# Kernel tuning notes

Hardware: AMD Instinct MI355X
Metric: run time of the kernel (lower is better)

The kernel has to match this reference:

```python
import jax, jax.numpy as jnp
import numpy as np

MAX_REL_POS = 16


def relative_position_ids(t, max_pos):
    r = jnp.arange(t)
    dist = jnp.clip(r[None, :] - r[:, None], -max_pos, max_pos)
    return dist + max_pos  # [T, T] in [0, 2*max_pos]


def setup_inputs():
    key = jax.random.key(0)
    ks = jax.random.split(key, 5)
    B, H, T, D = 2, 16, 1024, 64
    V = 2 * MAX_REL_POS + 1  # 33
    q = jax.random.normal(ks[0], (B, H, T, D), dtype=jnp.float32)
    k = jax.random.normal(ks[1], (B, H, T, D), dtype=jnp.float32)
    v = jax.random.normal(ks[2], (B, H, T, D), dtype=jnp.float32)
    embed_k = jax.random.normal(ks[3], (V, D), dtype=jnp.float32)
    embed_v = jax.random.normal(ks[4], (V, D), dtype=jnp.float32)
    mask = jnp.zeros((1, 1, T, T), dtype=jnp.float32)
    return {"q": q, "k": k, "v": v, "embed_k": embed_k, "embed_v": embed_v, "mask": mask}


def reference(q, k, v, embed_k, embed_v, mask):
    T = q.shape[2]
    D = k.shape[-1]
    rel = relative_position_ids(T, MAX_REL_POS)           # [T, T] int
    rel_k = embed_k[rel]                                   # [T, T, D]
    rel_v = embed_v[rel]                                   # [T, T, D]
    # QK^T plus relative-key term (matmul_with_relative_representations, transpose_b=True)
    logits = jnp.einsum('bhqd,bhkd->bhqk', q, k) + jnp.einsum('bhqd,qkd->bhqk', q, rel_k)
    logits = logits * (1.0 / jnp.sqrt(jnp.asarray(D, dtype=logits.dtype)))
    logits = logits + mask * (-1e9)
    attn = jax.nn.softmax(logits, axis=-1)                 # [B, H, T, T]
    out = jnp.einsum('bhqk,bhkd->bhqd', attn, v) + jnp.einsum('bhqk,qkd->bhqd', attn, rel_v)
    return out, attn
```

## Files before the change

### kernel.cpp

```cpp
#include <hip/hip_runtime.h>

#define BHN 32
#define T 1024
#define DD 64
#define TQ 16
#define PST 1032

typedef __attribute__((ext_vector_type(8))) __bf16 bf16x8;
typedef __attribute__((ext_vector_type(8))) unsigned short us8;
typedef __attribute__((ext_vector_type(4))) float f32x4;

struct alignas(16) U4 { unsigned a, b, c, d; };

__device__ __forceinline__ unsigned short f2bf(float x) {
  unsigned u = __builtin_bit_cast(unsigned, x);
  u += 0x7fffu + ((u >> 16) & 1u);
  return (unsigned short)(u >> 16);
}
__device__ __forceinline__ float bf2f(unsigned short h) {
  unsigned u = ((unsigned)h) << 16;
  return __builtin_bit_cast(float, u);
}
__device__ __forceinline__ bf16x8 ld_bf16x8(const unsigned short* p) {
  U4 u = *(const U4*)p;
  return __builtin_bit_cast(bf16x8, u);
}

__global__ __launch_bounds__(256) void prep_conv(
    const float* __restrict__ k, const float* __restrict__ v,
    unsigned short* __restrict__ kbf, unsigned short* __restrict__ vt)
{
  __shared__ float sT[64][66];
  const int bh = blockIdx.y;
  const int tb = blockIdx.x * 64;
  const int t = threadIdx.x;
  const size_t base = (size_t)bh * T * DD + (size_t)tb * DD;

  const float4* ksrc = (const float4*)(k + base);
#pragma unroll
  for (int i = 0; i < 2; ++i) {
    int g = i * 256 + t;
    float4 a = ksrc[g * 2], b = ksrc[g * 2 + 1];
    us8 u;
    u[0] = f2bf(a.x); u[1] = f2bf(a.y); u[2] = f2bf(a.z); u[3] = f2bf(a.w);
    u[4] = f2bf(b.x); u[5] = f2bf(b.y); u[6] = f2bf(b.z); u[7] = f2bf(b.w);
    *(us8*)(kbf + base + (size_t)g * 8) = u;
  }

  const float4* v4 = (const float4*)(v + base);
#pragma unroll
  for (int i = 0; i < 4; ++i) {
    int g = i * 256 + t;
    float4 x = v4[g];
    int tl = g >> 4;
    int d0 = (g & 15) * 4;
    sT[d0][tl] = x.x; sT[d0 + 1][tl] = x.y; sT[d0 + 2][tl] = x.z; sT[d0 + 3][tl] = x.w;
  }
  __syncthreads();

  unsigned short* vdst = vt + (size_t)bh * DD * T + tb;
#pragma unroll
  for (int i = 0; i < 2; ++i) {
    int item = i * 256 + t;
    int dd = item >> 3;
    int kk0 = (item & 7) * 8;
    float2 x0 = *(const float2*)&sT[dd][kk0];
    float2 x1 = *(const float2*)&sT[dd][kk0 + 2];
    float2 x2 = *(const float2*)&sT[dd][kk0 + 4];
    float2 x3 = *(const float2*)&sT[dd][kk0 + 6];
    us8 u;
    u[0] = f2bf(x0.x); u[1] = f2bf(x0.y); u[2] = f2bf(x1.x); u[3] = f2bf(x1.y);
    u[4] = f2bf(x2.x); u[5] = f2bf(x2.y); u[6] = f2bf(x3.x); u[7] = f2bf(x3.y);
    *(us8*)(vdst + (size_t)dd * T + kk0) = u;
  }
}

__global__ __launch_bounds__(256, 4) void attn_main(
    const float* __restrict__ q, const unsigned short* __restrict__ kbf,
    const unsigned short* __restrict__ vt, const float* __restrict__ ek,
    const float* __restrict__ ev, const float* __restrict__ mask,
    float* __restrict__ out, float* __restrict__ attn)
{
  __shared__ unsigned short sP[TQ * PST];
  __shared__ float sQek[TQ][33];
  __shared__ float sDiag[TQ][31];
  __shared__ float sRS[4][TQ];
  __shared__ float sRB[4][TQ];
  __shared__ float sInv[TQ];
  __shared__ float sB0n[TQ];

  const int bh = blockIdx.y;
  const int qb = blockIdx.x * TQ;
  const int tid = threadIdx.x;
  const int wave = tid >> 6;
  const int lane = tid & 63;
  const int quad = lane >> 4;
  const int col = lane & 15;

  for (int i = tid; i < TQ * 31; i += 256) (&sDiag[0][0])[i] = 0.f;

  const float* qrows = q + (size_t)bh * T * DD + (size_t)qb * DD;
  for (int idx = tid; idx < TQ * 33; idx += 256) {
    int i = idx / 33;
    int r = idx - i * 33;
    const float4* qa = (const float4*)(qrows + i * DD);
    const float4* eb = (const float4*)(ek + r * DD);
    float acc = 0.f;
#pragma unroll
    for (int d4 = 0; d4 < 16; ++d4) {
      float4 a = qa[d4], b = eb[d4];
      acc += a.x * b.x + a.y * b.y + a.z * b.z + a.w * b.w;
    }
    sQek[i][r] = acc;
  }

  bf16x8 aq0, aq1;
  {
    const float* qp = qrows + col * DD + quad * 8;
    float4 f0 = *(const float4*)(qp);
    float4 f1 = *(const float4*)(qp + 4);
    float4 f2 = *(const float4*)(qp + 32);
    float4 f3 = *(const float4*)(qp + 36);
    us8 u0, u1;
    u0[0] = f2bf(f0.x); u0[1] = f2bf(f0.y); u0[2] = f2bf(f0.z); u0[3] = f2bf(f0.w);
    u0[4] = f2bf(f1.x); u0[5] = f2bf(f1.y); u0[6] = f2bf(f1.z); u0[7] = f2bf(f1.w);
    u1[0] = f2bf(f2.x); u1[1] = f2bf(f2.y); u1[2] = f2bf(f2.z); u1[3] = f2bf(f2.w);
    u1[4] = f2bf(f3.x); u1[5] = f2bf(f3.y); u1[6] = f2bf(f3.z); u1[7] = f2bf(f3.w);
    aq0 = __builtin_bit_cast(bf16x8, u0);
    aq1 = __builtin_bit_cast(bf16x8, u1);
  }
  __syncthreads();

  float regS[4] = {0.f, 0.f, 0.f, 0.f};
  float regB[4] = {0.f, 0.f, 0.f, 0.f};
  const unsigned short* kbh = kbf + (size_t)bh * T * DD;
  const float* mrow = mask + (size_t)(qb + quad * 4) * T + col;

  float qe0r[4], qe32r[4];
#pragma unroll
  for (int r = 0; r < 4; ++r) {
    qe0r[r] = sQek[quad * 4 + r][0];
    qe32r[r] = sQek[quad * 4 + r][32];
  }

  int kt0 = wave * 256;
  const unsigned short* kp0 = kbh + (size_t)(kt0 + col) * DD + quad * 8;
  bf16x8 bk0 = ld_bf16x8(kp0);
  bf16x8 bk1 = ld_bf16x8(kp0 + 32);
  float mv0 = mrow[kt0], mv1 = mrow[T + kt0], mv2 = mrow[2 * T + kt0], mv3 = mrow[3 * T + kt0];

  for (int it = 0; it < 16; ++it) {
    const int ktc = wave * 256 + it * 16;
    const int ktn = wave * 256 + ((it + 1) & 15) * 16;
    const unsigned short* kpn = kbh + (size_t)(ktn + col) * DD + quad * 8;
    bf16x8 nk0 = ld_bf16x8(kpn);
    bf16x8 nk1 = ld_bf16x8(kpn + 32);
    float nm0 = mrow[ktn], nm1 = mrow[T + ktn], nm2 = mrow[2 * T + ktn], nm3 = mrow[3 * T + ktn];

    f32x4 acc = {0.f, 0.f, 0.f, 0.f};
    acc = __builtin_amdgcn_mfma_f32_16x16x32_bf16(aq0, bk0, acc, 0, 0, 0);
    acc = __builtin_amdgcn_mfma_f32_16x16x32_bf16(aq1, bk1, acc, 0, 0, 0);

    const int kg = ktc + col;
    unsigned short* spp = &sP[kg];
    const float mv[4] = {mv0, mv1, mv2, mv3};
    const int dkmax = ktc + 15 - qb;
    const int dkmin = ktc - qb - 15;

    if (dkmax < -16 || dkmin > 16) {
      const bool low = dkmax < -16;
#pragma unroll
      for (int r = 0; r < 4; ++r) {
        float qv = low ? qe0r[r] : qe32r[r];
        float logit = fmaf(mv[r], -1e9f, (acc[r] + qv) * 0.125f);
        float p = __expf(fminf(logit, 80.f));
        spp[(quad * 4 + r) * PST] = f2bf(p);
        regS[r] += p;
        if (low) regB[r] += p;
      }
    } else {
#pragma unroll
      for (int r = 0; r < 4; ++r) {
        int row = quad * 4 + r;
        int dk = kg - (qb + row);
        int rel = dk < -16 ? 0 : (dk > 16 ? 32 : dk + 16);
        float logit = fmaf(mv[r], -1e9f, (acc[r] + sQek[row][rel]) * 0.125f);
        float p = __expf(fminf(logit, 80.f));
        spp[row * PST] = f2bf(p);
        regS[r] += p;
        if (dk <= -16) regB[r] += p;
        if ((unsigned)(dk + 15) < 31u) sDiag[row][dk + 15] = p;
      }
    }
    bk0 = nk0; bk1 = nk1;
    mv0 = nm0; mv1 = nm1; mv2 = nm2; mv3 = nm3;
  }

#pragma unroll
  for (int r = 0; r < 4; ++r) {
    float s = regS[r], b = regB[r];
#pragma unroll
    for (int off = 1; off < 16; off <<= 1) {
      s += __shfl_xor(s, off, 64);
      b += __shfl_xor(b, off, 64);
    }
    if (col == 0) { sRS[wave][quad * 4 + r] = s; sRB[wave][quad * 4 + r] = b; }
  }
  __syncthreads();
  if (tid < TQ) {
    float S = sRS[0][tid] + sRS[1][tid] + sRS[2][tid] + sRS[3][tid];
    float B0 = sRB[0][tid] + sRB[1][tid] + sRB[2][tid] + sRB[3][tid];
    float inv = 1.f / S;
    sInv[tid] = inv;
    sB0n[tid] = B0 * inv;
  }

  const unsigned short* vtw = vt + (size_t)bh * DD * T + (size_t)(wave * 16 + col) * T + quad * 8;
  f32x4 oacc = {0.f, 0.f, 0.f, 0.f};
#pragma unroll 4
  for (int kc = 0; kc < 32; ++kc) {
    bf16x8 ap = ld_bf16x8(&sP[col * PST + kc * 32 + quad * 8]);
    bf16x8 bv = ld_bf16x8(vtw + kc * 32);
    oacc = __builtin_amdgcn_mfma_f32_16x16x32_bf16(ap, bv, oacc, 0, 0, 0);
  }
  __syncthreads();

  float* attnq = attn + (size_t)bh * T * T + (size_t)qb * T;
#pragma unroll 4
  for (int i = 0; i < 16; ++i) {
    float inv = sInv[i];
    ushort4 u = *(const ushort4*)&sP[i * PST + tid * 4];
    f32x4 o;
    o[0] = bf2f(u.x) * inv;
    o[1] = bf2f(u.y) * inv;
    o[2] = bf2f(u.z) * inv;
    o[3] = bf2f(u.w) * inv;
    __builtin_nontemporal_store(o, (f32x4*)(attnq + (size_t)i * T + tid * 4));
  }

  const int dcol = wave * 16 + col;
  float ev0 = ev[dcol];
  float ev32 = ev[32 * DD + dcol];
  float invr[4], accv[4];
#pragma unroll
  for (int r = 0; r < 4; ++r) {
    int row = quad * 4 + r;
    float inv = sInv[row];
    invr[r] = inv;
    float sumd = 0.f;
#pragma unroll
    for (int j = 0; j < 31; ++j) sumd += sDiag[row][j];
    float b0 = sB0n[row];
    float b32 = 1.f - b0 - sumd * inv;
    accv[r] = oacc[r] * inv + b0 * ev0 + b32 * ev32;
  }
  for (int j = 0; j < 31; ++j) {
    float e = ev[(j + 1) * DD + dcol];
#pragma unroll
    for (int r = 0; r < 4; ++r)
      accv[r] += sDiag[quad * 4 + r][j] * invr[r] * e;
  }
  float* outp = out + (size_t)bh * T * DD + (size_t)qb * DD;
#pragma unroll
  for (int r = 0; r < 4; ++r)
    outp[(size_t)(quad * 4 + r) * DD + dcol] = accv[r];
}

extern "C" void kernel_launch(void* const* d_in, const int* in_sizes, int n_in,
                              void* d_out, int out_size, void* d_ws, size_t ws_size,
                              hipStream_t stream) {
  const float* q    = (const float*)d_in[0];
  const float* k    = (const float*)d_in[1];
  const float* v    = (const float*)d_in[2];
  const float* ek   = (const float*)d_in[3];
  const float* ev   = (const float*)d_in[4];
  const float* mask = (const float*)d_in[5];

  float* out  = (float*)d_out;
  float* attn = out + (size_t)BHN * T * DD;

  unsigned short* kbf = (unsigned short*)d_ws;
  unsigned short* vt  = kbf + (size_t)BHN * T * DD;

  dim3 pg(T / 64, BHN);
  prep_conv<<<pg, 256, 0, stream>>>(k, v, kbf, vt);

  dim3 g(T / TQ, BHN);
  attn_main<<<g, 256, 0, stream>>>(q, kbf, vt, ek, ev, mask, out, attn);
}
```

Measured before the change: 279.1 us.

## Split fused attention kernel into QK and PV phases via global scratch

Splits the single attention kernel into a QK/softmax kernel and a PV kernel. The first kernel writes unnormalized bf16 probabilities into the first half of each fp32 attn row, plus per-row diagonal sums, inverse row sums and B0 into workspace. The second kernel reads them back, runs the PV MFMA from global memory, and writes the normalized fp32 attn rows in place. This aims to cut LDS pressure and raise occupancy per phase, at the cost of an extra kernel launch and an extra global round trip of the probabilities.

```diff
diff --git a/kernel.cpp b/kernel.cpp
--- a/kernel.cpp
+++ b/kernel.cpp
@@ -75,19 +75,17 @@
   }
 }
 
-__global__ __launch_bounds__(256, 4) void attn_main(
+__global__ __launch_bounds__(256, 4) void qk_phase(
     const float* __restrict__ q, const unsigned short* __restrict__ kbf,
-    const unsigned short* __restrict__ vt, const float* __restrict__ ek,
-    const float* __restrict__ ev, const float* __restrict__ mask,
-    float* __restrict__ out, float* __restrict__ attn)
+    const float* __restrict__ ek, const float* __restrict__ mask,
+    float* __restrict__ attn, float* __restrict__ diagG,
+    float* __restrict__ invG, float* __restrict__ b0G)
 {
   __shared__ unsigned short sP[TQ * PST];
   __shared__ float sQek[TQ][33];
-  __shared__ float sDiag[TQ][31];
+  __shared__ float sDiag[TQ][32];
   __shared__ float sRS[4][TQ];
   __shared__ float sRB[4][TQ];
-  __shared__ float sInv[TQ];
-  __shared__ float sB0n[TQ];
 
   const int bh = blockIdx.y;
   const int qb = blockIdx.x * TQ;
@@ -97,7 +95,8 @@
   const int quad = lane >> 4;
   const int col = lane & 15;
 
-  for (int i = tid; i < TQ * 31; i += 256) (&sDiag[0][0])[i] = 0.f;
+#pragma unroll
+  for (int i = 0; i < 2; ++i) (&sDiag[0][0])[i * 256 + tid] = 0.f;
 
   const float* qrows = q + (size_t)bh * T * DD + (size_t)qb * DD;
   for (int idx = tid; idx < TQ * 33; idx += 256) {
@@ -207,58 +206,107 @@
     if (col == 0) { sRS[wave][quad * 4 + r] = s; sRB[wave][quad * 4 + r] = b; }
   }
   __syncthreads();
+
+  const size_t growbase = (size_t)bh * T + qb;
   if (tid < TQ) {
     float S = sRS[0][tid] + sRS[1][tid] + sRS[2][tid] + sRS[3][tid];
     float B0 = sRB[0][tid] + sRB[1][tid] + sRB[2][tid] + sRB[3][tid];
-    float inv = 1.f / S;
-    sInv[tid] = inv;
-    sB0n[tid] = B0 * inv;
-  }
-
+    invG[growbase + tid] = 1.f / S;
+    b0G[growbase + tid] = B0;
+  }
+
+#pragma unroll
+  for (int i = 0; i < 8; ++i) {
+    int idx = i * 256 + tid;
+    int row = idx >> 7;
+    int g = idx & 127;
+    us8 val = *(const us8*)&sP[row * PST + g * 8];
+    *(us8*)((unsigned short*)(attn + (growbase + row) * (size_t)T) + g * 8) = val;
+  }
+
+#pragma unroll
+  for (int i = 0; i < 2; ++i) {
+    int idx = i * 256 + tid;
+    int row = idx >> 5;
+    int j = idx & 31;
+    diagG[(growbase + row) * 32 + j] = sDiag[row][j];
+  }
+}
+
+__global__ __launch_bounds__(256, 4) void pv_phase(
+    const unsigned short* __restrict__ vt, const float* __restrict__ ev,
+    float* __restrict__ attn, float* __restrict__ out,
+    const float* __restrict__ diagG, const float* __restrict__ invG,
+    const float* __restrict__ b0G)
+{
+  const int bh = blockIdx.y;
+  const int qb = blockIdx.x * TQ;
+  const int tid = threadIdx.x;
+  const int wave = tid >> 6;
+  const int lane = tid & 63;
+  const int quad = lane >> 4;
+  const int col = lane & 15;
+  const size_t growbase = (size_t)bh * T + qb;
+
+  const int g = tid & 127;
+  const int h = tid >> 7;
+  us8 src[8];
+#pragma unroll
+  for (int i = 0; i < 8; ++i) {
+    int row = 2 * i + h;
+    src[i] = __builtin_bit_cast(us8,
+        *(const U4*)((const unsigned short*)(attn + (growbase + row) * (size_t)T) + g * 8));
+  }
+
+  const unsigned short* pcol = (const unsigned short*)(attn + (growbase + col) * (size_t)T);
   const unsigned short* vtw = vt + (size_t)bh * DD * T + (size_t)(wave * 16 + col) * T + quad * 8;
   f32x4 oacc = {0.f, 0.f, 0.f, 0.f};
 #pragma unroll 4
   for (int kc = 0; kc < 32; ++kc) {
-    bf16x8 ap = ld_bf16x8(&sP[col * PST + kc * 32 + quad * 8]);
+    bf16x8 ap = ld_bf16x8(pcol + kc * 32 + quad * 8);
     bf16x8 bv = ld_bf16x8(vtw + kc * 32);
     oacc = __builtin_amdgcn_mfma_f32_16x16x32_bf16(ap, bv, oacc, 0, 0, 0);
   }
+
   __syncthreads();
 
-  float* attnq = attn + (size_t)bh * T * T + (size_t)qb * T;
-#pragma unroll 4
-  for (int i = 0; i < 16; ++i) {
-    float inv = sInv[i];
-    ushort4 u = *(const ushort4*)&sP[i * PST + tid * 4];
-    f32x4 o;
-    o[0] = bf2f(u.x) * inv;
-    o[1] = bf2f(u.y) * inv;
-    o[2] = bf2f(u.z) * inv;
-    o[3] = bf2f(u.w) * inv;
-    __builtin_nontemporal_store(o, (f32x4*)(attnq + (size_t)i * T + tid * 4));
+#pragma unroll
+  for (int i = 0; i < 8; ++i) {
+    int row = 2 * i + h;
+    float inv = invG[growbase + row];
+    float* dst = attn + (growbase + row) * (size_t)T + g * 8;
+    f32x4 o0, o1;
+    o0[0] = bf2f(src[i][0]) * inv; o0[1] = bf2f(src[i][1]) * inv;
+    o0[2] = bf2f(src[i][2]) * inv; o0[3] = bf2f(src[i][3]) * inv;
+    o1[0] = bf2f(src[i][4]) * inv; o1[1] = bf2f(src[i][5]) * inv;
+    o1[2] = bf2f(src[i][6]) * inv; o1[3] = bf2f(src[i][7]) * inv;
+    *(f32x4*)dst = o0;
+    *(f32x4*)(dst + 4) = o1;
   }
 
   const int dcol = wave * 16 + col;
   float ev0 = ev[dcol];
   float ev32 = ev[32 * DD + dcol];
-  float invr[4], accv[4];
+  float accv[4];
 #pragma unroll
   for (int r = 0; r < 4; ++r) {
     int row = quad * 4 + r;
-    float inv = sInv[row];
-    invr[r] = inv;
+    float inv = invG[growbase + row];
+    const float* drow = diagG + (growbase + row) * 32;
     float sumd = 0.f;
-#pragma unroll
-    for (int j = 0; j < 31; ++j) sumd += sDiag[row][j];
-    float b0 = sB0n[row];
-    float b32 = 1.f - b0 - sumd * inv;
-    accv[r] = oacc[r] * inv + b0 * ev0 + b32 * ev32;
-  }
-  for (int j = 0; j < 31; ++j) {
-    float e = ev[(j + 1) * DD + dcol];
-#pragma unroll
-    for (int r = 0; r < 4; ++r)
-      accv[r] += sDiag[quad * 4 + r][j] * invr[r] * e;
+    float rel = 0.f;
+#pragma unroll
+    for (int j4 = 0; j4 < 8; ++j4) {
+      float4 d = *(const float4*)(drow + j4 * 4);
+      sumd += d.x + d.y + d.z + d.w;
+      rel += d.x * ev[(j4 * 4 + 1) * DD + dcol];
+      rel += d.y * ev[(j4 * 4 + 2) * DD + dcol];
+      rel += d.z * ev[(j4 * 4 + 3) * DD + dcol];
+      rel += d.w * ev[(j4 * 4 + 4) * DD + dcol];
+    }
+    float b0 = b0G[growbase + row];
+    float b32 = 1.f - (b0 + sumd) * inv;
+    accv[r] = (oacc[r] + rel + b0 * ev0) * inv + b32 * ev32;
   }
   float* outp = out + (size_t)bh * T * DD + (size_t)qb * DD;
 #pragma unroll
@@ -281,10 +329,14 @@
 
   unsigned short* kbf = (unsigned short*)d_ws;
   unsigned short* vt  = kbf + (size_t)BHN * T * DD;
+  float* diagG = (float*)(vt + (size_t)BHN * DD * T);
+  float* invG  = diagG + (size_t)BHN * T * 32;
+  float* b0G   = invG + (size_t)BHN * T;
 
   dim3 pg(T / 64, BHN);
   prep_conv<<<pg, 256, 0, stream>>>(k, v, kbf, vt);
 
   dim3 g(T / TQ, BHN);
-  attn_main<<<g, 256, 0, stream>>>(q, kbf, vt, ek, ev, mask, out, attn);
-}
+  qk_phase<<<g, 256, 0, stream>>>(q, kbf, ek, mask, attn, diagG, invG, b0G);
+  pv_phase<<<g, 256, 0, stream>>>(vt, ev, attn, out, diagG, invG, b0G);
+}
```

Result: slower. 318.6 us (+14.1%).
